# Kernel tuning notes

Hardware: AMD Instinct MI355X
Metric: run time of the kernel (lower is better)

## Reference

```python
import jax, jax.numpy as jnp
import numpy as np

L, B, D = 512, 16, 256
H = 4            # MAX_DIFF == num_heads
MAX_BONDS = 6
MAX_DIFF = 4
PROB_SHIFT = 0.3


def _attn_weights(x, Wqk, Wq, bq, Wk, bk, mask):
    """Per-head softmax(QK^T/sqrt(hd)) with key padding mask.
    x: [b,l,d]; Wqk: [d,2d] (the inc/dec_qk pre-projection);
    Wq/Wk: [d,d] (MHA in_proj, stored x@W layout); mask: [b,l] bool (True=masked).
    Returns [b,h,l,l]. The V path / out_proj of the torch MHA are discarded
    by the original module, so they are omitted here.
    """
    b, l, d = x.shape
    hd = d // H
    q = x @ Wqk[:, :d]
    k = x @ Wqk[:, d:]
    Q = (q @ Wq + bq).reshape(b, l, H, hd)
    K = (k @ Wk + bk).reshape(b, l, H, hd)
    scores = jnp.einsum('blhd,bmhd->bhlm', Q, K) / np.sqrt(hd)
    scores = jnp.where(mask[:, None, None, :], -jnp.inf, scores)
    return jax.nn.softmax(scores, axis=-1)


def setup_inputs() -> dict:
    key = jax.random.key(0)
    ks = jax.random.split(key, 16)
    s = 0.05
    p = lambda k, shape: jax.random.normal(k, shape, jnp.float32) * s
    # key_padding_mask: last 64 positions padded (True == masked)
    src_mask = jnp.broadcast_to(jnp.arange(L)[None, :] >= (L - 64), (B, L))
    return {
        'molecule_embedding': jax.random.normal(ks[0], (L, B, D), jnp.float32),
        'src_bond': jax.random.randint(ks[1], (B, L, MAX_BONDS), 0, L, jnp.int32),
        'src_mask': src_mask,
        'W_inc_qk': p(ks[2], (D, 2 * D)),
        'Wq_inc': p(ks[3], (D, D)), 'bq_inc': p(ks[4], (D,)),
        'Wk_inc': p(ks[5], (D, D)), 'bk_inc': p(ks[6], (D,)),
        'W_dec_qk': p(ks[7], (D, 2 * D)),
        'Wq_dec': p(ks[8], (D, D)), 'bq_dec': p(ks[9], (D,)),
        'Wk_dec': p(ks[10], (D, D)), 'bk_dec': p(ks[11], (D,)),
        'Wc': p(ks[12], (MAX_DIFF, MAX_DIFF)), 'bc': p(ks[13], (MAX_DIFF,)),
    }


def reference(molecule_embedding, src_bond, src_mask,
              W_inc_qk, Wq_inc, bq_inc, Wk_inc, bk_inc,
              W_dec_qk, Wq_dec, bq_dec, Wk_dec, bk_dec,
              Wc, bc):
    x = jnp.transpose(molecule_embedding, (1, 0, 2))  # [b,l,d]
    b, l, _ = x.shape

    inc = _attn_weights(x, W_inc_qk, Wq_inc, bq_inc, Wk_inc, bk_inc, src_mask)
    dec = _attn_weights(x, W_dec_qk, Wq_dec, bq_dec, Wk_dec, bk_dec, src_mask)

    pad = (~src_mask).astype(jnp.float32)              # 1 - mask
    pm2 = pad[:, :, None] * pad[:, None, :]            # [b,l,l]

    # cls_layer((inc-dec).permute(0,2,3,1)) * (MAX_DIFF*pad_mask)[...,None]
    diff = (jnp.einsum('bhlm,hc->blmc', inc - dec, Wc) + bc)
    diff = diff * (MAX_DIFF * pm2)[..., None]          # [b,l,l,4]

    # src_bond has last dim == MAX_BONDS -> one-hot neighbor counts
    src_w = jax.nn.one_hot(src_bond, l, dtype=jnp.float32).sum(axis=2) * pm2  # [b,l,l]
    eye = jnp.eye(l, dtype=jnp.float32)
    src_w = src_w * (1.0 - eye)[None]                  # zero diagonal

    # _shift_probs(src_weight.long(), prob_shift, MAX_DIFF)
    oh = jax.nn.one_hot(src_w.astype(jnp.int32), MAX_DIFF, dtype=jnp.float32)
    probs = oh * (1.0 - PROB_SHIFT) + (1.0 - oh) * (PROB_SHIFT / (MAX_DIFF - 1))
    probs = probs / probs.sum(axis=-1, keepdims=True)

    return jnp.log(probs + 1e-6) + diff                # [b,l,l,4]
```

## Files before the change

kernel.cpp:

```cpp
#include <hip/hip_runtime.h>
#include <stdint.h>

typedef unsigned short u16t;
typedef short s8v __attribute__((ext_vector_type(8)));
typedef float f4v __attribute__((ext_vector_type(4)));

#define MFMA16 __builtin_amdgcn_mfma_f32_16x16x32_bf16
#define QKN (16*4*512*64)

__device__ __forceinline__ u16t f2bf(float f) {
  unsigned u = __builtin_bit_cast(unsigned, f);
  u += 0x7fffu + ((u >> 16) & 1u);
  return (u16t)(u >> 16);
}

__global__ __launch_bounds__(256) void prep_kernel(
    const float* __restrict__ Wiqk, const float* __restrict__ Wqi, const float* __restrict__ Wki,
    const float* __restrict__ Wdqk, const float* __restrict__ Wqd, const float* __restrict__ Wkd,
    u16t* __restrict__ weffT, const int* __restrict__ mraw, int* __restrict__ mdst) {
  __shared__ float At[16][65];
  __shared__ float Bt[16][65];
  __shared__ int mode;
  const int tid = threadIdx.x;

  if (blockIdx.z == 4) {
    if (tid == 0) mode = 0;
    __syncthreads();
    unsigned v0 = (unsigned)mraw[tid], v1 = (unsigned)mraw[tid + 256];
    if (v0 == 0x3F800000u || v1 == 0x3F800000u) mode = 2;
    __syncthreads();
    if (mode == 0 && (v0 > 1u || v1 > 1u)) mode = 1;
    __syncthreads();
    const int g = blockIdx.y * 4 + blockIdx.x;
#pragma unroll
    for (int i = 0; i < 2; ++i) {
      int idx = g * 512 + i * 256 + tid;
      int m;
      if (mode == 2)      m = (((const float*)mraw)[idx] != 0.0f) ? 1 : 0;
      else if (mode == 1) m = ((const unsigned char*)mraw)[idx];
      else                m = mraw[idx];
      mdst[idx] = m;
    }
    return;
  }

  const int n0 = blockIdx.x * 64;
  const int d0 = blockIdx.y * 64;
  const int p  = blockIdx.z;
  const float* A2  = (p == 0) ? Wqi : (p == 1) ? Wki : (p == 2) ? Wqd : Wkd;
  const float* Wqk = (p < 2) ? Wiqk : Wdqk;
  const int aoff = (p & 1) * 256;
  const int tx = tid & 15, ty = tid >> 4;

  float acc[4][4];
#pragma unroll
  for (int i = 0; i < 4; ++i)
#pragma unroll
    for (int j = 0; j < 4; ++j) acc[i][j] = 0.f;

  for (int k0 = 0; k0 < 256; k0 += 16) {
    __syncthreads();
    {
      int nn = tid & 63, kr = tid >> 6;
#pragma unroll
      for (int pass = 0; pass < 4; ++pass) {
        int kk = kr + pass * 4;
        At[kk][nn] = A2[(size_t)(k0 + kk) * 256 + n0 + nn];
      }
      int kk = tid & 15, dr = tid >> 4;
#pragma unroll
      for (int pass = 0; pass < 4; ++pass) {
        int dd = dr + pass * 16;
        Bt[kk][dd] = Wqk[(size_t)(d0 + dd) * 512 + aoff + k0 + kk];
      }
    }
    __syncthreads();
#pragma unroll
    for (int kk = 0; kk < 16; ++kk) {
      float a[4], b[4];
#pragma unroll
      for (int i = 0; i < 4; ++i) a[i] = At[kk][ty * 4 + i];
#pragma unroll
      for (int j = 0; j < 4; ++j) b[j] = Bt[kk][tx * 4 + j];
#pragma unroll
      for (int i = 0; i < 4; ++i)
#pragma unroll
        for (int j = 0; j < 4; ++j) acc[i][j] = fmaf(a[i], b[j], acc[i][j]);
    }
  }

#pragma unroll
  for (int i = 0; i < 4; ++i) {
    u16t h[4] = {f2bf(acc[i][0]), f2bf(acc[i][1]), f2bf(acc[i][2]), f2bf(acc[i][3])};
    *(uint2*)(&weffT[((size_t)(p * 256 + n0 + ty * 4 + i)) * 256 + d0 + tx * 4]) =
        *(const uint2*)h;
  }
}

__global__ __launch_bounds__(256) void proj_kernel(
    const float* __restrict__ emb, const u16t* __restrict__ weffT,
    const float* __restrict__ bq_inc, const float* __restrict__ bk_inc,
    const float* __restrict__ bq_dec, const float* __restrict__ bk_dec,
    u16t* __restrict__ qk) {
  __shared__ __align__(16) u16t As[128 * 40];
  __shared__ __align__(16) u16t Bs[128 * 40];
  const int t = threadIdx.x;
  const int f = (int)(blockIdx.x + gridDim.x * blockIdx.y);
  const int xcd = f & 7, idx = f >> 3;
  const int ry = xcd * 8 + (idx & 7);
  const int nx = idx >> 3;
  const int n0 = nx * 128;
  const int r0 = ry * 128;
  const int bb = r0 >> 9;
  const int l0 = r0 & 511;
  const int lane = t & 63, wid = t >> 6;
  const int quad = lane >> 4, c15 = lane & 15;
  const int wm = wid >> 1, wn = wid & 1;

  f4v acc[4][4];
#pragma unroll
  for (int i = 0; i < 4; ++i)
#pragma unroll
    for (int j = 0; j < 4; ++j) acc[i][j] = f4v{0.f, 0.f, 0.f, 0.f};

  for (int k0 = 0; k0 < 256; k0 += 32) {
    __syncthreads();
#pragma unroll
    for (int i = 0; i < 2; ++i) {
      int c = t + i * 256;
      int m = c >> 2, off = (c & 3) * 8;
      const float* src = emb + (size_t)((l0 + m) * 16 + bb) * 256 + k0 + off;
      float4 x0 = *(const float4*)src;
      float4 x1 = *(const float4*)(src + 4);
      unsigned p0, p1, p2, p3;
      asm("v_cvt_pk_bf16_f32 %0, %1, %2" : "=v"(p0) : "v"(x0.x), "v"(x0.y));
      asm("v_cvt_pk_bf16_f32 %0, %1, %2" : "=v"(p1) : "v"(x0.z), "v"(x0.w));
      asm("v_cvt_pk_bf16_f32 %0, %1, %2" : "=v"(p2) : "v"(x1.x), "v"(x1.y));
      asm("v_cvt_pk_bf16_f32 %0, %1, %2" : "=v"(p3) : "v"(x1.z), "v"(x1.w));
      uint4 pk = make_uint4(p0, p1, p2, p3);
      *(uint4*)(&As[m * 40 + off]) = pk;
      *(uint4*)(&Bs[m * 40 + off]) =
          *(const uint4*)(weffT + (size_t)(n0 + m) * 256 + k0 + off);
    }
    __syncthreads();
    s8v af[4], bf[4];
#pragma unroll
    for (int mi = 0; mi < 4; ++mi)
      af[mi] = *(const s8v*)(&As[(wm * 64 + mi * 16 + c15) * 40 + quad * 8]);
#pragma unroll
    for (int ni = 0; ni < 4; ++ni)
      bf[ni] = *(const s8v*)(&Bs[(wn * 64 + ni * 16 + c15) * 40 + quad * 8]);
#pragma unroll
    for (int mi = 0; mi < 4; ++mi)
#pragma unroll
      for (int ni = 0; ni < 4; ++ni)
        acc[mi][ni] = MFMA16(af[mi], bf[ni], acc[mi][ni], 0, 0, 0);
  }

  const float* biasP[4] = {bq_inc, bk_inc, bq_dec, bk_dec};
#pragma unroll
  for (int ni = 0; ni < 4; ++ni) {
    int n = n0 + wn * 64 + ni * 16 + c15;
    int p = n >> 8, h = (n >> 6) & 3, tt = n & 63, jj = n & 255;
    float bias = biasP[p][jj];
    u16t* dst = qk + (size_t)p * QKN;
#pragma unroll
    for (int mi = 0; mi < 4; ++mi) {
#pragma unroll
      for (int reg = 0; reg < 4; ++reg) {
        int l = l0 + wm * 64 + mi * 16 + quad * 4 + reg;
        dst[((size_t)(bb * 4 + h) * 512 + l) * 64 + tt] = f2bf(acc[mi][ni][reg] + bias);
      }
    }
  }
}

__global__ __launch_bounds__(512) void fused_kernel(
    const u16t* __restrict__ qk, const int* __restrict__ mask,
    const int* __restrict__ src_bond, const float* __restrict__ Wc,
    const float* __restrict__ bc, float* __restrict__ out) {
  __shared__ __align__(16) u16t Qs[8 * 16 * 72];
  __shared__ int bondsL[96];
  __shared__ int mlds[512 + 16];
  __shared__ __align__(16) float invL[8][16];
  __shared__ float wlds[16];
  const int t = threadIdx.x;

  const int f = (int)(blockIdx.x + gridDim.x * blockIdx.y);
  const int j = f >> 3;
  const int bb = (f & 7) * 2 + (j >> 5);
  const int l0 = (j & 31) * 16;

  const int lane = t & 63, wid = t >> 6;
  const int quad = lane >> 4, c15 = lane & 15;
  const int mbase = wid * 64 + c15;

#pragma unroll
  for (int i = 0; i < 2; ++i) {
    int c = t + i * 512;
    int q = c >> 7, row = (c >> 3) & 15, off = (c & 7) * 8;
    const u16t* Qb = qk + (size_t)(2 * (q >> 2)) * QKN;
    *(uint4*)(&Qs[(q * 16 + row) * 72 + off]) =
        *(const uint4*)(Qb + ((size_t)(bb * 4 + (q & 3)) * 512 + l0 + row) * 64 + off);
  }
  mlds[t] = mask[bb * 512 + t];
  if (t < 16) mlds[512 + t] = mask[bb * 512 + l0 + t];
  if (t < 96) bondsL[t] = src_bond[(size_t)(bb * 512 + l0 + t / 6) * 6 + (t % 6)];
  if (t >= 96 && t < 112) wlds[t - 96] = Wc[t - 96];

  __syncthreads();

  {
    const int q = wid;
    const int pp = q >> 2, h = q & 3;
    const u16t* Kb = qk + (size_t)(2 * pp + 1) * QKN + (size_t)(bb * 4 + h) * 512 * 64;
    s8v a0 = *(const s8v*)(&Qs[(q * 16 + c15) * 72 + quad * 8]);
    s8v a1 = *(const s8v*)(&Qs[(q * 16 + c15) * 72 + 32 + quad * 8]);
    float rs[4] = {0.f, 0.f, 0.f, 0.f};
#pragma unroll 4
    for (int tt = 0; tt < 32; ++tt) {
      const u16t* row = Kb + (size_t)(tt * 16 + c15) * 64 + quad * 8;
      s8v k0 = *(const s8v*)row;
      s8v k1 = *(const s8v*)(row + 32);
      f4v s = f4v{0.f, 0.f, 0.f, 0.f};
      s = MFMA16(a0, k0, s, 0, 0, 0);
      s = MFMA16(a1, k1, s, 0, 0, 0);
      bool msk = (mlds[tt * 16 + c15] != 0);
#pragma unroll
      for (int reg = 0; reg < 4; ++reg)
        rs[reg] += msk ? 0.f : __expf(s[reg] * 0.125f);
    }
#pragma unroll
    for (int reg = 0; reg < 4; ++reg) {
#pragma unroll
      for (int off = 1; off < 16; off <<= 1) rs[reg] += __shfl_xor(rs[reg], off);
    }
    const float sgn = (q >= 4) ? -1.f : 1.f;
    if (c15 == 0) {
#pragma unroll
      for (int reg = 0; reg < 4; ++reg) invL[q][quad * 4 + reg] = sgn / rs[reg];
    }
  }

  s8v kb0[4], kb1[4];
  {
    const u16t* Kb = qk + (size_t)1 * QKN + (size_t)(bb * 4) * 512 * 64;
#pragma unroll
    for (int nt = 0; nt < 4; ++nt) {
      const u16t* row = Kb + (size_t)(mbase + nt * 16) * 64 + quad * 8;
      kb0[nt] = *(const s8v*)row;
      kb1[nt] = *(const s8v*)(row + 32);
    }
  }

  __syncthreads();

  bool mskm[4];
#pragma unroll
  for (int nt = 0; nt < 4; ++nt) mskm[nt] = (mlds[mbase + nt * 16] != 0);

  float dacc[4][4][4];
#pragma unroll
  for (int nt = 0; nt < 4; ++nt)
#pragma unroll
    for (int r = 0; r < 4; ++r)
#pragma unroll
      for (int c = 0; c < 4; ++c) dacc[nt][r][c] = 0.f;

#pragma unroll 1
  for (int q = 0; q < 8; ++q) {
    const int h = q & 3;
    s8v a0 = *(const s8v*)(&Qs[(q * 16 + c15) * 72 + quad * 8]);
    s8v a1 = *(const s8v*)(&Qs[(q * 16 + c15) * 72 + 32 + quad * 8]);
    f4v ivv = *(const f4v*)&invL[q][quad * 4];
    float wv[4];
#pragma unroll
    for (int c = 0; c < 4; ++c) wv[c] = wlds[h * 4 + c];

    f4v s[4];
#pragma unroll
    for (int nt = 0; nt < 4; ++nt) {
      f4v sacc = f4v{0.f, 0.f, 0.f, 0.f};
      sacc = MFMA16(a0, kb0[nt], sacc, 0, 0, 0);
      sacc = MFMA16(a1, kb1[nt], sacc, 0, 0, 0);
      s[nt] = sacc;
    }

    if (q < 7) {
      const int qn = q + 1;
      const u16t* Kb = qk + (size_t)(2 * (qn >> 2) + 1) * QKN
                          + (size_t)(bb * 4 + (qn & 3)) * 512 * 64;
#pragma unroll
      for (int nt = 0; nt < 4; ++nt) {
        const u16t* row = Kb + (size_t)(mbase + nt * 16) * 64 + quad * 8;
        kb0[nt] = *(const s8v*)row;
        kb1[nt] = *(const s8v*)(row + 32);
      }
    }

#pragma unroll
    for (int nt = 0; nt < 4; ++nt) {
#pragma unroll
      for (int reg = 0; reg < 4; ++reg) {
        float e = mskm[nt] ? 0.f : __expf(s[nt][reg] * 0.125f);
        float P = e * ivv[reg];
#pragma unroll
        for (int c = 0; c < 4; ++c)
          dacc[nt][reg][c] = fmaf(P, wv[c], dacc[nt][reg][c]);
      }
    }
  }

  float bcF[4];
#pragma unroll
  for (int c = 0; c < 4; ++c) bcF[c] = bc[c];
  const float lgH = logf(0.7f + 1e-6f);
  const float lgM = logf(0.1f + 1e-6f);
  const float lgU = logf(0.25f + 1e-6f);

#pragma unroll
  for (int nt = 0; nt < 4; ++nt) {
    int m = mbase + nt * 16;
    bool padm = !mskm[nt];
#pragma unroll
    for (int reg = 0; reg < 4; ++reg) {
      int lloc = quad * 4 + reg;
      int l = l0 + lloc;
      bool padl = (mlds[512 + lloc] == 0);
      bool pm = padl && padm;
      int cnt = 0;
#pragma unroll
      for (int j6 = 0; j6 < 6; ++j6) cnt += (bondsL[lloc * 6 + j6] == m) ? 1 : 0;
      int cls = (pm && (m != l)) ? cnt : 0;
      float v[4];
#pragma unroll
      for (int c = 0; c < 4; ++c) {
        float lp = (cls >= 4) ? lgU : ((c == cls) ? lgH : lgM);
        float dv = pm ? 4.f * (dacc[nt][reg][c] + bcF[c]) : 0.f;
        v[c] = lp + dv;
      }
      float4 o = make_float4(v[0], v[1], v[2], v[3]);
      *(float4*)(&out[((size_t)(bb * 512 + l) * 512 + m) * 4]) = o;
    }
  }
}

extern "C" void kernel_launch(void* const* d_in, const int* in_sizes, int n_in,
                              void* d_out, int out_size, void* d_ws, size_t ws_size,
                              hipStream_t stream) {
  (void)in_sizes; (void)n_in; (void)out_size; (void)ws_size;
  const float* emb      = (const float*)d_in[0];
  const int*   src_bond = (const int*)d_in[1];
  const int*   mask_raw = (const int*)d_in[2];
  const float* W_inc_qk = (const float*)d_in[3];
  const float* Wq_inc   = (const float*)d_in[4];
  const float* bq_inc   = (const float*)d_in[5];
  const float* Wk_inc   = (const float*)d_in[6];
  const float* bk_inc   = (const float*)d_in[7];
  const float* W_dec_qk = (const float*)d_in[8];
  const float* Wq_dec   = (const float*)d_in[9];
  const float* bq_dec   = (const float*)d_in[10];
  const float* Wk_dec   = (const float*)d_in[11];
  const float* bk_dec   = (const float*)d_in[12];
  const float* Wc       = (const float*)d_in[13];
  const float* bc       = (const float*)d_in[14];
  float* out = (float*)d_out;

  char* ws = (char*)d_ws;
  int*   wsMask = (int*)ws;
  u16t*  weffT  = (u16t*)(ws + 32768);
  u16t*  qk     = (u16t*)(ws + 32768 + 524288);

  hipLaunchKernelGGL(prep_kernel, dim3(4, 4, 5), dim3(256), 0, stream,
                     W_inc_qk, Wq_inc, Wk_inc, W_dec_qk, Wq_dec, Wk_dec, weffT,
                     mask_raw, wsMask);
  hipLaunchKernelGGL(proj_kernel, dim3(8, 64), dim3(256), 0, stream,
                     emb, weffT, bq_inc, bk_inc, bq_dec, bk_dec, qk);
  hipLaunchKernelGGL(fused_kernel, dim3(32, 16), dim3(512), 0, stream,
                     qk, wsMask, src_bond, Wc, bc, out);
}
```

Baseline: 201.8 us.

## Split softmax row-sum pass into separate stats kernel and fold scale into projection

The per-row softmax denominator computation moves out of the fused kernel into a new stats kernel. It runs on a 1024-block grid, uses DPP row reductions and a fast reciprocal, and writes inverse sums to workspace. The 1/sqrt(hd) scale is folded into the Q projection output, which removes a multiply per exp. The final kernel now loads K fragments directly per head instead of prefetching them one head ahead. This adds a kernel launch and an invsum round trip through global memory in exchange for better parallelism in the stats phase and a shorter critical path in the main kernel.

Measured after the change: 206.4 us. 2.3% more time.

```diff
diff --git a/kernel.cpp b/kernel.cpp
--- a/kernel.cpp
+++ b/kernel.cpp
@@ -12,6 +12,19 @@
   unsigned u = __builtin_bit_cast(unsigned, f);
   u += 0x7fffu + ((u >> 16) & 1u);
   return (u16t)(u >> 16);
+}
+
+__device__ __forceinline__ float rowred16(float x) {
+  int t;
+  t = __builtin_amdgcn_update_dpp(0, __builtin_bit_cast(int, x), 0x128, 0xf, 0xf, false);
+  x += __builtin_bit_cast(float, t);
+  t = __builtin_amdgcn_update_dpp(0, __builtin_bit_cast(int, x), 0x124, 0xf, 0xf, false);
+  x += __builtin_bit_cast(float, t);
+  t = __builtin_amdgcn_update_dpp(0, __builtin_bit_cast(int, x), 0x122, 0xf, 0xf, false);
+  x += __builtin_bit_cast(float, t);
+  t = __builtin_amdgcn_update_dpp(0, __builtin_bit_cast(int, x), 0x121, 0xf, 0xf, false);
+  x += __builtin_bit_cast(float, t);
+  return x;
 }
 
 __global__ __launch_bounds__(256) void prep_kernel(
@@ -163,22 +176,71 @@
     int n = n0 + wn * 64 + ni * 16 + c15;
     int p = n >> 8, h = (n >> 6) & 3, tt = n & 63, jj = n & 255;
     float bias = biasP[p][jj];
+    const float osc = (p & 1) ? 1.0f : 0.125f;
     u16t* dst = qk + (size_t)p * QKN;
 #pragma unroll
     for (int mi = 0; mi < 4; ++mi) {
 #pragma unroll
       for (int reg = 0; reg < 4; ++reg) {
         int l = l0 + wm * 64 + mi * 16 + quad * 4 + reg;
-        dst[((size_t)(bb * 4 + h) * 512 + l) * 64 + tt] = f2bf(acc[mi][ni][reg] + bias);
-      }
-    }
-  }
-}
-
-__global__ __launch_bounds__(512) void fused_kernel(
+        dst[((size_t)(bb * 4 + h) * 512 + l) * 64 + tt] =
+            f2bf((acc[mi][ni][reg] + bias) * osc);
+      }
+    }
+  }
+}
+
+__global__ __launch_bounds__(256) void stats2_kernel(
     const u16t* __restrict__ qk, const int* __restrict__ mask,
-    const int* __restrict__ src_bond, const float* __restrict__ Wc,
-    const float* __restrict__ bc, float* __restrict__ out) {
+    float* __restrict__ invsum) {
+  const int t = threadIdx.x;
+  const int f = (int)blockIdx.x;
+  const int q = f & 7;
+  const int idx = f >> 3;
+  const int bb = idx >> 3;
+  const int lg = idx & 7;
+  const int lane = t & 63, wid = t >> 6;
+  const int l0 = (lg * 4 + wid) * 16;
+  const int quad = lane >> 4, c15 = lane & 15;
+  const int pp = q >> 2, h = q & 3;
+
+  const u16t* Qp = qk + (size_t)(2 * pp) * QKN
+                      + ((size_t)(bb * 4 + h) * 512 + l0 + c15) * 64 + quad * 8;
+  s8v a0 = *(const s8v*)Qp;
+  s8v a1 = *(const s8v*)(Qp + 32);
+  const u16t* Kb = qk + (size_t)(2 * pp + 1) * QKN + (size_t)(bb * 4 + h) * 512 * 64;
+  const int* mrow = mask + bb * 512;
+
+  float rs[4] = {0.f, 0.f, 0.f, 0.f};
+#pragma unroll 4
+  for (int tt = 0; tt < 32; ++tt) {
+    const u16t* kr = Kb + (size_t)(tt * 16 + c15) * 64 + quad * 8;
+    s8v k0 = *(const s8v*)kr;
+    s8v k1 = *(const s8v*)(kr + 32);
+    f4v s = f4v{0.f, 0.f, 0.f, 0.f};
+    s = MFMA16(a0, k0, s, 0, 0, 0);
+    s = MFMA16(a1, k1, s, 0, 0, 0);
+    bool msk = (mrow[tt * 16 + c15] != 0);
+#pragma unroll
+    for (int reg = 0; reg < 4; ++reg)
+      rs[reg] += msk ? 0.f : __expf(s[reg]);
+  }
+#pragma unroll
+  for (int reg = 0; reg < 4; ++reg) rs[reg] = rowred16(rs[reg]);
+  const float sgn = (q >= 4) ? -1.f : 1.f;
+  if (c15 == 0) {
+#pragma unroll
+    for (int reg = 0; reg < 4; ++reg)
+      invsum[((size_t)q * 16 + bb) * 512 + l0 + quad * 4 + reg] =
+          sgn * __builtin_amdgcn_rcpf(rs[reg]);
+  }
+}
+
+__global__ __launch_bounds__(512) void final_kernel(
+    const u16t* __restrict__ qk, const int* __restrict__ mask,
+    const float* __restrict__ invsum, const int* __restrict__ src_bond,
+    const float* __restrict__ Wc, const float* __restrict__ bc,
+    float* __restrict__ out) {
   __shared__ __align__(16) u16t Qs[8 * 16 * 72];
   __shared__ int bondsL[96];
   __shared__ int mlds[512 + 16];
@@ -194,6 +256,8 @@
   const int lane = t & 63, wid = t >> 6;
   const int quad = lane >> 4, c15 = lane & 15;
   const int mbase = wid * 64 + c15;
+  const u16t* Kblk = qk + (size_t)(bb * 4) * 512 * 64;
+  const int loff = mbase * 64 + quad * 8;
 
 #pragma unroll
   for (int i = 0; i < 2; ++i) {
@@ -207,50 +271,9 @@
   if (t < 16) mlds[512 + t] = mask[bb * 512 + l0 + t];
   if (t < 96) bondsL[t] = src_bond[(size_t)(bb * 512 + l0 + t / 6) * 6 + (t % 6)];
   if (t >= 96 && t < 112) wlds[t - 96] = Wc[t - 96];
-
-  __syncthreads();
-
-  {
-    const int q = wid;
-    const int pp = q >> 2, h = q & 3;
-    const u16t* Kb = qk + (size_t)(2 * pp + 1) * QKN + (size_t)(bb * 4 + h) * 512 * 64;
-    s8v a0 = *(const s8v*)(&Qs[(q * 16 + c15) * 72 + quad * 8]);
-    s8v a1 = *(const s8v*)(&Qs[(q * 16 + c15) * 72 + 32 + quad * 8]);
-    float rs[4] = {0.f, 0.f, 0.f, 0.f};
-#pragma unroll 4
-    for (int tt = 0; tt < 32; ++tt) {
-      const u16t* row = Kb + (size_t)(tt * 16 + c15) * 64 + quad * 8;
-      s8v k0 = *(const s8v*)row;
-      s8v k1 = *(const s8v*)(row + 32);
-      f4v s = f4v{0.f, 0.f, 0.f, 0.f};
-      s = MFMA16(a0, k0, s, 0, 0, 0);
-      s = MFMA16(a1, k1, s, 0, 0, 0);
-      bool msk = (mlds[tt * 16 + c15] != 0);
-#pragma unroll
-      for (int reg = 0; reg < 4; ++reg)
-        rs[reg] += msk ? 0.f : __expf(s[reg] * 0.125f);
-    }
-#pragma unroll
-    for (int reg = 0; reg < 4; ++reg) {
-#pragma unroll
-      for (int off = 1; off < 16; off <<= 1) rs[reg] += __shfl_xor(rs[reg], off);
-    }
-    const float sgn = (q >= 4) ? -1.f : 1.f;
-    if (c15 == 0) {
-#pragma unroll
-      for (int reg = 0; reg < 4; ++reg) invL[q][quad * 4 + reg] = sgn / rs[reg];
-    }
-  }
-
-  s8v kb0[4], kb1[4];
-  {
-    const u16t* Kb = qk + (size_t)1 * QKN + (size_t)(bb * 4) * 512 * 64;
-#pragma unroll
-    for (int nt = 0; nt < 4; ++nt) {
-      const u16t* row = Kb + (size_t)(mbase + nt * 16) * 64 + quad * 8;
-      kb0[nt] = *(const s8v*)row;
-      kb1[nt] = *(const s8v*)(row + 32);
-    }
+  if (t >= 128 && t < 256) {
+    int q = (t - 128) >> 4, lr = (t - 128) & 15;
+    invL[q][lr] = invsum[((size_t)q * 16 + bb) * 512 + l0 + lr];
   }
 
   __syncthreads();
@@ -272,38 +295,24 @@
     const int h = q & 3;
     s8v a0 = *(const s8v*)(&Qs[(q * 16 + c15) * 72 + quad * 8]);
     s8v a1 = *(const s8v*)(&Qs[(q * 16 + c15) * 72 + 32 + quad * 8]);
-    f4v ivv = *(const f4v*)&invL[q][quad * 4];
+    f4v iv = *(const f4v*)(&invL[q][quad * 4]);
     float wv[4];
 #pragma unroll
     for (int c = 0; c < 4; ++c) wv[c] = wlds[h * 4 + c];
 
-    f4v s[4];
+    const u16t* Kq = Kblk + (size_t)(2 * (q >> 2) + 1) * QKN
+                          + (size_t)(q & 3) * (512 * 64);
 #pragma unroll
     for (int nt = 0; nt < 4; ++nt) {
+      s8v k0 = *(const s8v*)(Kq + loff + nt * 1024);
+      s8v k1 = *(const s8v*)(Kq + loff + nt * 1024 + 32);
       f4v sacc = f4v{0.f, 0.f, 0.f, 0.f};
-      sacc = MFMA16(a0, kb0[nt], sacc, 0, 0, 0);
-      sacc = MFMA16(a1, kb1[nt], sacc, 0, 0, 0);
-      s[nt] = sacc;
-    }
-
-    if (q < 7) {
-      const int qn = q + 1;
-      const u16t* Kb = qk + (size_t)(2 * (qn >> 2) + 1) * QKN
-                          + (size_t)(bb * 4 + (qn & 3)) * 512 * 64;
-#pragma unroll
-      for (int nt = 0; nt < 4; ++nt) {
-        const u16t* row = Kb + (size_t)(mbase + nt * 16) * 64 + quad * 8;
-        kb0[nt] = *(const s8v*)row;
-        kb1[nt] = *(const s8v*)(row + 32);
-      }
-    }
-
-#pragma unroll
-    for (int nt = 0; nt < 4; ++nt) {
+      sacc = MFMA16(a0, k0, sacc, 0, 0, 0);
+      sacc = MFMA16(a1, k1, sacc, 0, 0, 0);
 #pragma unroll
       for (int reg = 0; reg < 4; ++reg) {
-        float e = mskm[nt] ? 0.f : __expf(s[nt][reg] * 0.125f);
-        float P = e * ivv[reg];
+        float e = mskm[nt] ? 0.f : __expf(sacc[reg]);
+        float P = e * iv[reg];
 #pragma unroll
         for (int c = 0; c < 4; ++c)
           dacc[nt][reg][c] = fmaf(P, wv[c], dacc[nt][reg][c]);
@@ -370,12 +379,15 @@
   int*   wsMask = (int*)ws;
   u16t*  weffT  = (u16t*)(ws + 32768);
   u16t*  qk     = (u16t*)(ws + 32768 + 524288);
+  float* invsum = (float*)(ws + 32768 + 524288 + 16777216);
 
   hipLaunchKernelGGL(prep_kernel, dim3(4, 4, 5), dim3(256), 0, stream,
                      W_inc_qk, Wq_inc, Wk_inc, W_dec_qk, Wq_dec, Wk_dec, weffT,
                      mask_raw, wsMask);
   hipLaunchKernelGGL(proj_kernel, dim3(8, 64), dim3(256), 0, stream,
                      emb, weffT, bq_inc, bk_inc, bq_dec, bk_dec, qk);
-  hipLaunchKernelGGL(fused_kernel, dim3(32, 16), dim3(512), 0, stream,
-                     qk, wsMask, src_bond, Wc, bc, out);
-}
+  hipLaunchKernelGGL(stats2_kernel, dim3(1024), dim3(256), 0, stream,
+                     qk, wsMask, invsum);
+  hipLaunchKernelGGL(final_kernel, dim3(32, 16), dim3(512), 0, stream,
+                     qk, wsMask, invsum, src_bond, Wc, bc, out);
+}
```
